# Kernel optimization log

Measured on AMD Instinct MI355X. Metric: run time of the kernel, lower is better.

Reference implementation:

```python
import jax, jax.numpy as jnp
import numpy as np

N_NODES = 50000
N_EDGES = 800000
IN_DIM = 128
HID = 32
HEADS = 4


def _lin_init(key, fan_in, fan_out):
    k1, k2 = jax.random.split(key)
    s = 1.0 / np.sqrt(fan_in)
    W = jax.random.uniform(k1, (fan_in, fan_out), jnp.float32, -s, s)
    b = jax.random.uniform(k2, (fan_out,), jnp.float32, -s, s)
    return W, b


def setup_inputs() -> dict:
    key = jax.random.key(0)
    keys = jax.random.split(key, 12)
    x = jax.random.normal(keys[0], (N_NODES, IN_DIM), jnp.float32)
    edge_index = jax.random.randint(keys[1], (2, N_EDGES), 0, N_NODES, jnp.int64)

    # conv1: in_dim -> heads*hid (128 -> 4*32)
    Wq1, bq1 = _lin_init(keys[2], IN_DIM, HEADS * HID)
    Wk1, bk1 = _lin_init(keys[3], IN_DIM, HEADS * HID)
    Wv1, bv1 = _lin_init(keys[4], IN_DIM, HEADS * HID)
    Ws1, bs1 = _lin_init(keys[5], IN_DIM, HEADS * HID)
    # conv2: 128 -> 1*32
    Wq2, bq2 = _lin_init(keys[6], HEADS * HID, HID)
    Wk2, bk2 = _lin_init(keys[7], HEADS * HID, HID)
    Wv2, bv2 = _lin_init(keys[8], HEADS * HID, HID)
    Ws2, bs2 = _lin_init(keys[9], HEADS * HID, HID)
    # output linear: 32 -> 1
    Wo, bo = _lin_init(keys[10], HID, 1)

    return {
        "x": x, "edge_index": edge_index,
        "Wq1": Wq1, "bq1": bq1, "Wk1": Wk1, "bk1": bk1,
        "Wv1": Wv1, "bv1": bv1, "Ws1": Ws1, "bs1": bs1,
        "Wq2": Wq2, "bq2": bq2, "Wk2": Wk2, "bk2": bk2,
        "Wv2": Wv2, "bv2": bv2, "Ws2": Ws2, "bs2": bs2,
        "Wo": Wo, "bo": bo,
    }


def transformer_conv(x, edge_index, Wq, bq, Wk, bk, Wv, bv, Ws, bs, heads, d):
    # PyG TransformerConv (concat=True, root_weight=True, beta=False, no edge attr).
    n = x.shape[0]
    src, dst = edge_index[0], edge_index[1]  # message j(src) -> i(dst)
    q = (x @ Wq + bq).reshape(n, heads, d)
    k = (x @ Wk + bk).reshape(n, heads, d)
    v = (x @ Wv + bv).reshape(n, heads, d)
    # per-edge attention logits [E, heads]
    logits = (q[dst] * k[src]).sum(-1) / jnp.sqrt(jnp.float32(d))
    # segment softmax over incoming edges of each target node
    m = jax.ops.segment_max(logits, dst, num_segments=n)
    p = jnp.exp(logits - m[dst])
    denom = jax.ops.segment_sum(p, dst, num_segments=n)
    alpha = p / denom[dst]  # [E, heads]
    # weighted scatter-add of values
    msg = alpha[:, :, None] * v[src]  # [E, heads, d]
    aggr = jax.ops.segment_sum(msg, dst, num_segments=n).reshape(n, heads * d)
    return aggr + x @ Ws + bs  # root (skip) connection


def reference(x, edge_index,
              Wq1, bq1, Wk1, bk1, Wv1, bv1, Ws1, bs1,
              Wq2, bq2, Wk2, bk2, Wv2, bv2, Ws2, bs2,
              Wo, bo):
    h = transformer_conv(x, edge_index, Wq1, bq1, Wk1, bk1, Wv1, bv1, Ws1, bs1, HEADS, HID)
    h = jax.nn.relu(h)
    h = transformer_conv(h, edge_index, Wq2, bq2, Wk2, bk2, Wv2, bv2, Ws2, bs2, 1, HID)
    h = jax.nn.relu(h)
    g = h.mean(axis=0)  # [HID]
    return g @ Wo + bo  # [1]
```

## Files before the change

kernel.cpp:

```cpp
#include <hip/hip_runtime.h>
#include <math.h>

#define N_NODES 50000
#define N_EDGES 800000
#define NBK 196
#define BCAP 6144

typedef short short8 __attribute__((ext_vector_type(8)));
typedef float f32x4 __attribute__((ext_vector_type(4)));
typedef float f32x2 __attribute__((ext_vector_type(2)));

__device__ inline unsigned short f2bf(float v) {
  unsigned u = __float_as_uint(v);
  u += 0x7FFFu + ((u >> 16) & 1u);
  return (unsigned short)(u >> 16);
}
__device__ inline float bf2f(unsigned short b) {
  return __uint_as_float(((unsigned)b) << 16);
}
__device__ inline float bflo(unsigned u) { return __uint_as_float(u << 16); }
__device__ inline float bfhi(unsigned u) { return __uint_as_float(u & 0xFFFF0000u); }
__device__ inline unsigned char f2fp8(float v) {
  return (unsigned char)(__builtin_amdgcn_cvt_pk_fp8_f32(v, 0.f, 0, false) & 0xFF);
}
template <bool HI>
__device__ inline f32x2 fp8dec(unsigned u) {
  return __builtin_amdgcn_cvt_pk_f32_fp8(u, HI);
}

#define SCL 0.17677669529663687f

#define CAST_B 6250
#define C1_B 256
#define C2_B 64
__global__ void prep_fused(const float* __restrict__ x,
                           const float* __restrict__ Wq1, const float* __restrict__ Wk1,
                           const float* __restrict__ Wv1, const float* __restrict__ Ws1,
                           const float* __restrict__ bq1, const float* __restrict__ bk1,
                           const float* __restrict__ bv1, const float* __restrict__ bs1,
                           const float* __restrict__ Wq2, const float* __restrict__ Wk2,
                           const float* __restrict__ Wv2, const float* __restrict__ Ws2,
                           const float* __restrict__ bq2, const float* __restrict__ bk2,
                           const float* __restrict__ bv2, const float* __restrict__ bs2,
                           unsigned short* __restrict__ xb, unsigned short* __restrict__ Wt1,
                           float* __restrict__ bcat1, unsigned short* __restrict__ Wt2,
                           float* __restrict__ bcat2, int* __restrict__ bhist,
                           float* __restrict__ ACC) {
  const int b = blockIdx.x, tid = threadIdx.x;
  if (b < CAST_B) {
    int i = b * 256 + tid;
    float4 v = ((const float4*)x)[i];
    ushort4 o;
    o.x = f2bf(v.x); o.y = f2bf(v.y); o.z = f2bf(v.z); o.w = f2bf(v.w);
    ((ushort4*)xb)[i] = o;
  } else if (b < CAST_B + C1_B) {
    int i = (b - CAST_B) * 256 + tid;
    int c = i >> 7, k = i & 127;
    int mi = c >> 7, lc = c & 127;
    const float* W = (mi == 0) ? Wq1 : (mi == 1) ? Wk1 : (mi == 2) ? Wv1 : Ws1;
    float scl = (mi == 0) ? SCL : 1.f;
    Wt1[i] = f2bf(W[(size_t)k * 128 + lc] * scl);
    if (i < 512) {
      int bm = i >> 7, bl = i & 127;
      const float* bb = (bm == 0) ? bq1 : (bm == 1) ? bk1 : (bm == 2) ? bv1 : bs1;
      bcat1[i] = bb[bl] * ((bm == 0) ? SCL : 1.f);
    }
  } else if (b < CAST_B + C1_B + C2_B) {
    int i = (b - CAST_B - C1_B) * 256 + tid;
    int c = i >> 7, k = i & 127;
    int mi = c >> 5, lc = c & 31;
    const float* W = (mi == 0) ? Wq2 : (mi == 1) ? Wk2 : (mi == 2) ? Wv2 : Ws2;
    float scl = (mi == 0) ? SCL : 1.f;
    Wt2[i] = f2bf(W[(size_t)k * 32 + lc] * scl);
    if (i < 128) {
      int bm = i >> 5, bl = i & 31;
      const float* bb = (bm == 0) ? bq2 : (bm == 1) ? bk2 : (bm == 2) ? bv2 : bs2;
      bcat2[i] = bb[bl] * ((bm == 0) ? SCL : 1.f);
    }
  } else {
    if (tid < NBK) bhist[tid] = 0;
    else if (tid >= 224 && tid < 256) ACC[tid - 224] = 0.f;
  }
}

__global__ __launch_bounds__(256) void gemm_conv1(
    const unsigned short* __restrict__ Ab, const unsigned short* __restrict__ Wt,
    const float* __restrict__ bcat, unsigned short* __restrict__ Q1b,
    unsigned short* __restrict__ SK1, unsigned char* __restrict__ KV8, int M) {
  __shared__ __align__(16) unsigned char Lsb[64 * 272];
  unsigned short* Ls16 = (unsigned short*)Lsb;
  const int bm = blockIdx.x * 64;
  const int tid = threadIdx.x, wave = tid >> 6, lane = tid & 63;
  const int lr = lane & 15, q = lane >> 4;

  if (blockIdx.y < 2) {
    const int coloff = blockIdx.y ? 384 : 0;
    unsigned short* out = blockIdx.y ? SK1 : Q1b;
    f32x4 acc[4][2];
#pragma unroll
    for (int i = 0; i < 4; ++i)
#pragma unroll
      for (int j = 0; j < 2; ++j) acc[i][j] = (f32x4){0.f, 0.f, 0.f, 0.f};
#pragma unroll
    for (int ks = 0; ks < 4; ++ks) {
      short8 af[4], bf[2];
#pragma unroll
      for (int i = 0; i < 4; ++i) {
        int gm = bm + i * 16 + lr; if (gm >= M) gm = 0;
        af[i] = *(const short8*)(Ab + (size_t)gm * 128 + ks * 32 + q * 8);
      }
#pragma unroll
      for (int j = 0; j < 2; ++j)
        bf[j] = *(const short8*)(Wt + (size_t)(coloff + wave * 32 + j * 16 + lr) * 128 + ks * 32 + q * 8);
#pragma unroll
      for (int i = 0; i < 4; ++i)
#pragma unroll
        for (int j = 0; j < 2; ++j)
          acc[i][j] = __builtin_amdgcn_mfma_f32_16x16x32_bf16(af[i], bf[j], acc[i][j], 0, 0, 0);
    }
    float bj[2];
#pragma unroll
    for (int j = 0; j < 2; ++j) bj[j] = bcat[coloff + wave * 32 + j * 16 + lr];
#pragma unroll
    for (int i = 0; i < 4; ++i)
#pragma unroll
      for (int r = 0; r < 4; ++r) {
        int row = i * 16 + q * 4 + r;
#pragma unroll
        for (int j = 0; j < 2; ++j) {
          int c = wave * 32 + j * 16 + lr;
          Ls16[row * 136 + c] = f2bf(acc[i][j][r] + bj[j]);
        }
      }
    __syncthreads();
#pragma unroll
    for (int p = 0; p < 8; ++p) {
      int idx = tid + p * 256;
      int row = idx >> 5, u = idx & 31;
      int gr = bm + row;
      if (gr < M) *(uint2*)(out + (size_t)gr * 128 + u * 4) = *(const uint2*)&Ls16[row * 136 + u * 4];
    }
  } else {
    f32x4 acc[4][4];
#pragma unroll
    for (int i = 0; i < 4; ++i)
#pragma unroll
      for (int j = 0; j < 4; ++j) acc[i][j] = (f32x4){0.f, 0.f, 0.f, 0.f};
#pragma unroll
    for (int ks = 0; ks < 4; ++ks) {
      short8 af[4], bf[4];
#pragma unroll
      for (int i = 0; i < 4; ++i) {
        int gm = bm + i * 16 + lr; if (gm >= M) gm = 0;
        af[i] = *(const short8*)(Ab + (size_t)gm * 128 + ks * 32 + q * 8);
      }
#pragma unroll
      for (int j = 0; j < 4; ++j)
        bf[j] = *(const short8*)(Wt + (size_t)(128 + wave * 64 + j * 16 + lr) * 128 + ks * 32 + q * 8);
#pragma unroll
      for (int i = 0; i < 4; ++i)
#pragma unroll
        for (int j = 0; j < 4; ++j)
          acc[i][j] = __builtin_amdgcn_mfma_f32_16x16x32_bf16(af[i], bf[j], acc[i][j], 0, 0, 0);
    }
    float bj[4];
#pragma unroll
    for (int j = 0; j < 4; ++j) bj[j] = bcat[128 + wave * 64 + j * 16 + lr];
#pragma unroll
    for (int i = 0; i < 4; ++i)
#pragma unroll
      for (int r = 0; r < 4; ++r) {
        int row = i * 16 + q * 4 + r;
#pragma unroll
        for (int j = 0; j < 4; ++j) {
          int c = wave * 64 + j * 16 + lr;
          int bslot = (c < 128) ? (4 * (c >> 1) + (c & 1))
                                : (4 * ((c - 128) >> 1) + 2 + ((c - 128) & 1));
          Lsb[row * 272 + bslot] = f2fp8(acc[i][j][r] + bj[j]);
        }
      }
    __syncthreads();
#pragma unroll
    for (int p = 0; p < 16; ++p) {
      int idx = tid + p * 256;
      int row = idx >> 6, u = idx & 63;
      int gr = bm + row;
      if (gr < M) *(unsigned*)(KV8 + (size_t)gr * 256 + u * 4) = *(const unsigned*)&Lsb[row * 272 + u * 4];
    }
  }
}

__global__ __launch_bounds__(256) void gemm2(
    const unsigned short* __restrict__ Ab, const unsigned short* __restrict__ Wt,
    const float* __restrict__ bcat, unsigned char* __restrict__ C2b, int M) {
  __shared__ __align__(16) unsigned char Lsb[64 * 272];
  const int bm = blockIdx.x * 64;
  const int tid = threadIdx.x, wave = tid >> 6, lane = tid & 63;
  const int lr = lane & 15, q = lane >> 4;

  f32x4 acc[4][2];
#pragma unroll
  for (int i = 0; i < 4; ++i)
#pragma unroll
    for (int j = 0; j < 2; ++j) acc[i][j] = (f32x4){0.f, 0.f, 0.f, 0.f};

#pragma unroll
  for (int ks = 0; ks < 4; ++ks) {
    short8 af[4], bf[2];
#pragma unroll
    for (int i = 0; i < 4; ++i) {
      int gm = bm + i * 16 + lr; if (gm >= M) gm = 0;
      af[i] = *(const short8*)(Ab + (size_t)gm * 128 + ks * 32 + q * 8);
    }
#pragma unroll
    for (int j = 0; j < 2; ++j)
      bf[j] = *(const short8*)(Wt + (size_t)(wave * 32 + j * 16 + lr) * 128 + ks * 32 + q * 8);
#pragma unroll
    for (int i = 0; i < 4; ++i)
#pragma unroll
      for (int j = 0; j < 2; ++j)
        acc[i][j] = __builtin_amdgcn_mfma_f32_16x16x32_bf16(af[i], bf[j], acc[i][j], 0, 0, 0);
  }

  float bj[2];
#pragma unroll
  for (int j = 0; j < 2; ++j) bj[j] = bcat[wave * 32 + j * 16 + lr];
#pragma unroll
  for (int i = 0; i < 4; ++i)
#pragma unroll
    for (int r = 0; r < 4; ++r) {
      int row = i * 16 + q * 4 + r;
#pragma unroll
      for (int j = 0; j < 2; ++j) {
        int c = wave * 32 + j * 16 + lr;
        float val = acc[i][j][r] + bj[j];
        if (c < 32) {
          *(unsigned short*)&Lsb[row * 272 + 2 * c] = f2bf(val);
        } else if (c < 64) {
          int d = c - 32;
          Lsb[row * 272 + 64 + 4 * (d >> 1) + (d & 1)] = f2fp8(val);
        } else if (c < 96) {
          int d = c - 64;
          Lsb[row * 272 + 64 + 4 * (d >> 1) + 2 + (d & 1)] = f2fp8(val);
        } else {
          *(unsigned short*)&Lsb[row * 272 + 192 + 2 * (c - 96)] = f2bf(val);
        }
      }
    }
  __syncthreads();
#pragma unroll
  for (int p = 0; p < 16; ++p) {
    int idx = tid + p * 256;
    int row = idx >> 6, u = idx & 63;
    int gr = bm + row;
    if (gr < M) *(unsigned*)(C2b + (size_t)gr * 256 + u * 4) = *(const unsigned*)&Lsb[row * 272 + u * 4];
  }
}

__global__ void bucket_hist(const int* __restrict__ ei, int* __restrict__ bhist, int E) {
  __shared__ int h[NBK];
  for (int i = threadIdx.x; i < NBK; i += 256) h[i] = 0;
  __syncthreads();
  int e = blockIdx.x * 4096 + threadIdx.x;
#pragma unroll
  for (int p = 0; p < 16; ++p, e += 256)
    if (e < E) atomicAdd(&h[ei[E + e] >> 8], 1);
  __syncthreads();
  for (int i = threadIdx.x; i < NBK; i += 256)
    if (h[i]) atomicAdd(&bhist[i], h[i]);
}

__global__ void bucket_scan(const int* __restrict__ bhist, int* __restrict__ boff,
                            int* __restrict__ bcur) {
  __shared__ int s[256];
  int t = threadIdx.x;
  int v = (t < NBK) ? bhist[t] : 0;
  s[t] = v;
  __syncthreads();
#pragma unroll
  for (int off = 1; off < 256; off <<= 1) {
    int u = (t >= off) ? s[t - off] : 0;
    __syncthreads();
    s[t] += u;
    __syncthreads();
  }
  if (t < NBK) {
    int excl = s[t] - v;
    boff[t] = excl;
    bcur[t] = excl;
  }
  if (t == NBK - 1) boff[NBK] = s[t];
}

__global__ void bucket_scatter(const int* __restrict__ ei, int* __restrict__ bcur,
                               int2* __restrict__ ebuck, int E) {
  __shared__ int lh[NBK];
  for (int i = threadIdx.x; i < NBK; i += 256) lh[i] = 0;
  __syncthreads();
  const int e0 = blockIdx.x * 4096;
  int srcs[16], dsts[16];
#pragma unroll
  for (int p = 0; p < 16; ++p) {
    int e = e0 + p * 256 + threadIdx.x;
    if (e < E) {
      srcs[p] = ei[e];
      dsts[p] = ei[E + e];
      atomicAdd(&lh[dsts[p] >> 8], 1);
    } else dsts[p] = -1;
  }
  __syncthreads();
  for (int i = threadIdx.x; i < NBK; i += 256)
    if (lh[i]) lh[i] = atomicAdd(&bcur[i], lh[i]);
  __syncthreads();
#pragma unroll
  for (int p = 0; p < 16; ++p) {
    if (dsts[p] >= 0) {
      int slot = atomicAdd(&lh[dsts[p] >> 8], 1);
      ebuck[slot] = make_int2(srcs[p], dsts[p]);
    }
  }
}

__global__ void bucket_csr(const int2* __restrict__ ebuck, const int* __restrict__ boff,
                           int* __restrict__ rowptr, int* __restrict__ esrc, int N) {
  const int b = blockIdx.x;
  const int lo = boff[b], hi = boff[b + 1];
  const int cnt = hi - lo;
  __shared__ int hist[256];
  __shared__ int cur[256];
  __shared__ int sorted[BCAP];
  const int t = threadIdx.x;
  hist[t] = 0;
  __syncthreads();
  for (int i = t; i < cnt; i += 256) {
    int2 ed = ebuck[lo + i];
    atomicAdd(&hist[ed.y & 255], 1);
  }
  __syncthreads();
  int v = hist[t];
  sorted[t] = v;
  __syncthreads();
#pragma unroll
  for (int off = 1; off < 256; off <<= 1) {
    int u = (t >= off) ? sorted[t - off] : 0;
    __syncthreads();
    sorted[t] += u;
    __syncthreads();
  }
  int excl = sorted[t] - v;
  cur[t] = excl;
  int node = b * 256 + t;
  if (node <= N) rowptr[node] = lo + excl;
  __syncthreads();
  for (int i = t; i < cnt; i += 256) {
    int2 ed = ebuck[lo + i];
    int slot = atomicAdd(&cur[ed.y & 255], 1);
    if (slot < BCAP) sorted[slot] = ed.x;
    else esrc[lo + slot] = ed.x << 8;
  }
  __syncthreads();
  int lim = cnt < BCAP ? cnt : BCAP;
  for (int i = t; i < lim; i += 256) esrc[lo + i] = sorted[i] << 8;
}

__global__ void node_attn1(const int* __restrict__ rowptr, const int* __restrict__ esrc,
                           const unsigned short* __restrict__ Qb,
                           const unsigned char* __restrict__ KV8,
                           const unsigned short* __restrict__ SK, unsigned short* __restrict__ Hb,
                           int n) {
  int node = (blockIdx.x * blockDim.x + threadIdx.x) >> 6;
  int lane = threadIdx.x & 63;
  if (node >= n) return;
  const int half = lane >> 5, ll = lane & 31;
  const int r0 = rowptr[node], r1 = rowptr[node + 1];
  uint2 qq = *(const uint2*)(Qb + (size_t)node * 128 + ll * 4);
  const float q0 = bflo(qq.x), q1 = bfhi(qq.x), q2 = bflo(qq.y), q3 = bfhi(qq.y);
  float l = 0.f, a0 = 0.f, a1 = 0.f, a2 = 0.f, a3 = 0.f;
  const unsigned char* kvb = KV8 + ll * 8;
  int j = r0;
  for (; j + 8 <= r1; j += 8) {
    int e = j + half * 4;
    int s0 = esrc[e], s1 = esrc[e + 1], s2 = esrc[e + 2], s3 = esrc[e + 3];
    uint2 u0 = *(const uint2*)(kvb + s0);
    uint2 u1 = *(const uint2*)(kvb + s1);
    uint2 u2 = *(const uint2*)(kvb + s2);
    uint2 u3 = *(const uint2*)(kvb + s3);
    f32x2 k0a = fp8dec<false>(u0.x), k0b = fp8dec<false>(u0.y);
    f32x2 k1a = fp8dec<false>(u1.x), k1b = fp8dec<false>(u1.y);
    f32x2 k2a = fp8dec<false>(u2.x), k2b = fp8dec<false>(u2.y);
    f32x2 k3a = fp8dec<false>(u3.x), k3b = fp8dec<false>(u3.y);
    float d0 = q0 * k0a.x + q1 * k0a.y + q2 * k0b.x + q3 * k0b.y;
    float d1 = q0 * k1a.x + q1 * k1a.y + q2 * k1b.x + q3 * k1b.y;
    float d2 = q0 * k2a.x + q1 * k2a.y + q2 * k2b.x + q3 * k2b.y;
    float d3 = q0 * k3a.x + q1 * k3a.y + q2 * k3b.x + q3 * k3b.y;
#pragma unroll
    for (int msk = 1; msk <= 4; msk <<= 1) {
      d0 += __shfl_xor(d0, msk);
      d1 += __shfl_xor(d1, msk);
      d2 += __shfl_xor(d2, msk);
      d3 += __shfl_xor(d3, msk);
    }
    float p0 = __expf(d0), p1 = __expf(d1), p2 = __expf(d2), p3 = __expf(d3);
    l += (p0 + p1) + (p2 + p3);
    f32x2 v0a = fp8dec<true>(u0.x), v0b = fp8dec<true>(u0.y);
    f32x2 v1a = fp8dec<true>(u1.x), v1b = fp8dec<true>(u1.y);
    f32x2 v2a = fp8dec<true>(u2.x), v2b = fp8dec<true>(u2.y);
    f32x2 v3a = fp8dec<true>(u3.x), v3b = fp8dec<true>(u3.y);
    a0 += p0 * v0a.x + p1 * v1a.x + p2 * v2a.x + p3 * v3a.x;
    a1 += p0 * v0a.y + p1 * v1a.y + p2 * v2a.y + p3 * v3a.y;
    a2 += p0 * v0b.x + p1 * v1b.x + p2 * v2b.x + p3 * v3b.x;
    a3 += p0 * v0b.y + p1 * v1b.y + p2 * v2b.y + p3 * v3b.y;
  }
  for (; j < r1; j += 4) {
    int eA = j + half * 2, eB = eA + 1;
    bool vA = eA < r1, vB = eB < r1;
    int sA = esrc[vA ? eA : r0];
    int sB = esrc[vB ? eB : r0];
    uint2 ua = *(const uint2*)(kvb + sA);
    uint2 ub = *(const uint2*)(kvb + sB);
    f32x2 ka1 = fp8dec<false>(ua.x), ka2 = fp8dec<false>(ua.y);
    f32x2 kb1 = fp8dec<false>(ub.x), kb2 = fp8dec<false>(ub.y);
    float dA = q0 * ka1.x + q1 * ka1.y + q2 * ka2.x + q3 * ka2.y;
    float dB = q0 * kb1.x + q1 * kb1.y + q2 * kb2.x + q3 * kb2.y;
#pragma unroll
    for (int msk = 1; msk <= 4; msk <<= 1) {
      dA += __shfl_xor(dA, msk);
      dB += __shfl_xor(dB, msk);
    }
    float pA = vA ? __expf(dA) : 0.f;
    float pB = vB ? __expf(dB) : 0.f;
    l += pA + pB;
    f32x2 va1 = fp8dec<true>(ua.x), va2 = fp8dec<true>(ua.y);
    f32x2 vb1 = fp8dec<true>(ub.x), vb2 = fp8dec<true>(ub.y);
    a0 += pA * va1.x + pB * vb1.x;
    a1 += pA * va1.y + pB * vb1.y;
    a2 += pA * va2.x + pB * vb2.x;
    a3 += pA * va2.y + pB * vb2.y;
  }
  l  += __shfl_xor(l, 32);
  a0 += __shfl_xor(a0, 32);
  a1 += __shfl_xor(a1, 32);
  a2 += __shfl_xor(a2, 32);
  a3 += __shfl_xor(a3, 32);
  float inv = (l > 0.f) ? 1.f / l : 0.f;
  if (half == 0) {
    uint2 sk = *(const uint2*)(SK + (size_t)node * 128 + ll * 4);
    float o0 = fmaxf(bflo(sk.x) + a0 * inv, 0.f);
    float o1 = fmaxf(bfhi(sk.x) + a1 * inv, 0.f);
    float o2 = fmaxf(bflo(sk.y) + a2 * inv, 0.f);
    float o3 = fmaxf(bfhi(sk.y) + a3 * inv, 0.f);
    uint2 hb;
    hb.x = ((unsigned)f2bf(o1) << 16) | (unsigned)f2bf(o0);
    hb.y = ((unsigned)f2bf(o3) << 16) | (unsigned)f2bf(o2);
    *(uint2*)(Hb + (size_t)node * 128 + ll * 4) = hb;
  }
}

__global__ void node_attn2(const int* __restrict__ rowptr, const int* __restrict__ esrc,
                           unsigned char* __restrict__ C2b, int n) {
  int node = (blockIdx.x * blockDim.x + threadIdx.x) >> 6;
  int lane = threadIdx.x & 63;
  if (node >= n) return;
  const int g = lane >> 4, gl = lane & 15;
  const int r0 = rowptr[node], r1 = rowptr[node + 1];
  unsigned qu = *(const unsigned*)(C2b + (size_t)node * 256 + gl * 4);
  const float q0 = bflo(qu), q1 = bfhi(qu);
  float l = 0.f, a0 = 0.f, a1 = 0.f;
  const unsigned char* kvb = C2b + 64 + gl * 4;
  int j = r0;
  for (; j + 8 <= r1; j += 8) {
    int e = j + g * 2;
    int s0 = esrc[e], s1 = esrc[e + 1];
    unsigned u0 = *(const unsigned*)(kvb + s0);
    unsigned u1 = *(const unsigned*)(kvb + s1);
    f32x2 k0 = fp8dec<false>(u0), k1 = fp8dec<false>(u1);
    float d0 = q0 * k0.x + q1 * k0.y;
    float d1 = q0 * k1.x + q1 * k1.y;
#pragma unroll
    for (int msk = 1; msk <= 8; msk <<= 1) {
      d0 += __shfl_xor(d0, msk);
      d1 += __shfl_xor(d1, msk);
    }
    float p0 = __expf(d0), p1 = __expf(d1);
    l += p0 + p1;
    f32x2 v0 = fp8dec<true>(u0), v1 = fp8dec<true>(u1);
    a0 += p0 * v0.x + p1 * v1.x;
    a1 += p0 * v0.y + p1 * v1.y;
  }
  for (; j < r1; j += 4) {
    bool v = (j + g) < r1;
    int s = esrc[v ? j + g : r0];
    unsigned u = *(const unsigned*)(kvb + s);
    f32x2 kd = fp8dec<false>(u);
    float d = q0 * kd.x + q1 * kd.y;
#pragma unroll
    for (int msk = 1; msk <= 8; msk <<= 1) d += __shfl_xor(d, msk);
    float p = v ? __expf(d) : 0.f;
    l += p;
    f32x2 vd = fp8dec<true>(u);
    a0 += p * vd.x;
    a1 += p * vd.y;
  }
#pragma unroll
  for (int msk = 16; msk <= 32; msk <<= 1) {
    l  += __shfl_xor(l, msk);
    a0 += __shfl_xor(a0, msk);
    a1 += __shfl_xor(a1, msk);
  }
  float inv = (l > 0.f) ? 1.f / l : 0.f;
  if (lane < 16) {
    unsigned* h = (unsigned*)(C2b + (size_t)node * 256 + 192 + gl * 4);
    unsigned hu = *h;
    float o0 = bflo(hu) + a0 * inv;
    float o1 = bfhi(hu) + a1 * inv;
    *h = ((unsigned)f2bf(o1) << 16) | (unsigned)f2bf(o0);
  }
}

__global__ void mean_reduce(const unsigned char* __restrict__ C2b, float* __restrict__ ACC, int n) {
  __shared__ float s[256];
  float acc = 0.f;
  int stride = gridDim.x * blockDim.x;
  int total = n * 32;
  for (int i = blockIdx.x * blockDim.x + threadIdx.x; i < total; i += stride) {
    int node = i >> 5, c = i & 31;
    unsigned short h = *(const unsigned short*)(C2b + (size_t)node * 256 + 192 + c * 2);
    acc += fmaxf(bf2f(h), 0.f);
  }
  s[threadIdx.x] = acc;
  __syncthreads();
  for (int off = 128; off >= 32; off >>= 1) {
    if (threadIdx.x < off) s[threadIdx.x] += s[threadIdx.x + off];
    __syncthreads();
  }
  if (threadIdx.x < 32) atomicAdd(&ACC[threadIdx.x], s[threadIdx.x]);
}

__global__ void final_out(const float* __restrict__ ACC, const float* __restrict__ Wo,
                          const float* __restrict__ bo, float* __restrict__ out, float invN) {
  int lane = threadIdx.x;
  float v = 0.f;
  if (lane < 32) v = ACC[lane] * invN * Wo[lane];
  v += __shfl_xor(v, 1);
  v += __shfl_xor(v, 2);
  v += __shfl_xor(v, 4);
  v += __shfl_xor(v, 8);
  v += __shfl_xor(v, 16);
  v += __shfl_xor(v, 32);
  if (lane == 0) out[0] = v + bo[0];
}

extern "C" void kernel_launch(void* const* d_in, const int* in_sizes, int n_in,
                              void* d_out, int out_size, void* d_ws, size_t ws_size,
                              hipStream_t stream) {
  const float* x   = (const float*)d_in[0];
  const int*   ei  = (const int*)d_in[1];
  const float* Wq1 = (const float*)d_in[2];  const float* bq1 = (const float*)d_in[3];
  const float* Wk1 = (const float*)d_in[4];  const float* bk1 = (const float*)d_in[5];
  const float* Wv1 = (const float*)d_in[6];  const float* bv1 = (const float*)d_in[7];
  const float* Ws1 = (const float*)d_in[8];  const float* bs1 = (const float*)d_in[9];
  const float* Wq2 = (const float*)d_in[10]; const float* bq2 = (const float*)d_in[11];
  const float* Wk2 = (const float*)d_in[12]; const float* bk2 = (const float*)d_in[13];
  const float* Wv2 = (const float*)d_in[14]; const float* bv2 = (const float*)d_in[15];
  const float* Ws2 = (const float*)d_in[16]; const float* bs2 = (const float*)d_in[17];
  const float* Wo  = (const float*)d_in[18]; const float* bo  = (const float*)d_in[19];

  char* ws = (char*)d_ws;
  const int N = N_NODES, E = N_EDGES;
  const int GB = (N + 63) / 64;
  const int EB = (E + 4095) / 4096;

  unsigned short* xb  = (unsigned short*)(ws + 0);
  unsigned short* Q1b = (unsigned short*)(ws + 12800000);
  unsigned short* SK1 = (unsigned short*)(ws + 25600000);
  unsigned char*  KV1 = (unsigned char*)(ws + 38400000);
  unsigned short* H1b = (unsigned short*)(ws + 64000000);
  unsigned char*  C2  = (unsigned char*)(ws + 76800000);
  int* rowptr = (int*)(ws + 102400000);
  int* esrc   = (int*)(ws + 102700032);
  int* bhist  = (int*)(ws + 105900032);
  int* boff   = (int*)(ws + 105901056);
  int* bcur   = (int*)(ws + 105902080);
  unsigned short* Wt1   = (unsigned short*)(ws + 105903104);
  unsigned short* Wt2   = (unsigned short*)(ws + 106034176);
  float*          bcat1 = (float*)(ws + 106066944);
  float*          bcat2 = (float*)(ws + 106068992);
  float*          ACC   = (float*)(ws + 106069504);
  int2*           ebuck = (int2*)(ws + 106070016);

  float* out = (float*)d_out;

  dim3 blk(256);

  prep_fused<<<dim3(CAST_B + C1_B + C2_B + 1), blk, 0, stream>>>(
      x, Wq1, Wk1, Wv1, Ws1, bq1, bk1, bv1, bs1,
      Wq2, Wk2, Wv2, Ws2, bq2, bk2, bv2, bs2,
      xb, Wt1, bcat1, Wt2, bcat2, bhist, ACC);

  bucket_hist<<<dim3(EB), blk, 0, stream>>>(ei, bhist, E);
  bucket_scan<<<dim3(1), blk, 0, stream>>>(bhist, boff, bcur);
  bucket_scatter<<<dim3(EB), blk, 0, stream>>>(ei, bcur, ebuck, E);
  bucket_csr<<<dim3(NBK), blk, 0, stream>>>(ebuck, boff, rowptr, esrc, N);

  gemm_conv1<<<dim3(GB, 3), blk, 0, stream>>>(xb, Wt1, bcat1, Q1b, SK1, KV1, N);

  node_attn1<<<dim3((N * 64 + 255) / 256), blk, 0, stream>>>(rowptr, esrc, Q1b, KV1, SK1, H1b, N);

  gemm2<<<dim3(GB), blk, 0, stream>>>(H1b, Wt2, bcat2, C2, N);

  node_attn2<<<dim3((N * 64 + 255) / 256), blk, 0, stream>>>(rowptr, esrc, C2, N);

  mean_reduce<<<dim3(1024), blk, 0, stream>>>(C2, ACC, N);
  final_out<<<dim3(1), dim3(64), 0, stream>>>(ACC, Wo, bo, out, 1.0f / (float)N);
}
```

Before: 284.3 us.

## Merge conv1 GEMM column blocks into one block and stage A tile in LDS

The conv1 projection GEMM now runs one block per 64-row tile instead of three blocks along y. Each wave computes 128 output columns (Q, K, V or skip), and the A tile is loaded once into shared memory and reused across all 512 columns. The conv2 GEMM stages its A tile in LDS the same way. This removes repeated global reads of x rows and widens the output stores, at the cost of more accumulator registers per wave (32 f32x4), roughly three times the LDS per block, and a third as many blocks.

Measured after the change: 270.4 us. 4.9% less time.

```diff
diff --git a/kernel.cpp b/kernel.cpp
--- a/kernel.cpp
+++ b/kernel.cpp
@@ -87,105 +87,86 @@
     const unsigned short* __restrict__ Ab, const unsigned short* __restrict__ Wt,
     const float* __restrict__ bcat, unsigned short* __restrict__ Q1b,
     unsigned short* __restrict__ SK1, unsigned char* __restrict__ KV8, int M) {
-  __shared__ __align__(16) unsigned char Lsb[64 * 272];
-  unsigned short* Ls16 = (unsigned short*)Lsb;
+  __shared__ __align__(16) unsigned char L[3][64 * 272];
+  unsigned short* As = (unsigned short*)L[0];
   const int bm = blockIdx.x * 64;
   const int tid = threadIdx.x, wave = tid >> 6, lane = tid & 63;
   const int lr = lane & 15, q = lane >> 4;
 
-  if (blockIdx.y < 2) {
-    const int coloff = blockIdx.y ? 384 : 0;
-    unsigned short* out = blockIdx.y ? SK1 : Q1b;
-    f32x4 acc[4][2];
+#pragma unroll
+  for (int p = 0; p < 4; ++p) {
+    int f = tid + p * 256;
+    int row = f >> 4, chunk = f & 15;
+    int gm = bm + row; if (gm >= M) gm = 0;
+    uint4 v = *(const uint4*)(Ab + (size_t)gm * 128 + chunk * 8);
+    *(uint4*)&As[row * 136 + chunk * 8] = v;
+  }
+  __syncthreads();
+
+  const int colbase = wave * 128;
+  f32x4 acc[4][8];
+#pragma unroll
+  for (int i = 0; i < 4; ++i)
+#pragma unroll
+    for (int j = 0; j < 8; ++j) acc[i][j] = (f32x4){0.f, 0.f, 0.f, 0.f};
+
+#pragma unroll
+  for (int ks = 0; ks < 4; ++ks) {
+    short8 af[4];
 #pragma unroll
     for (int i = 0; i < 4; ++i)
-#pragma unroll
-      for (int j = 0; j < 2; ++j) acc[i][j] = (f32x4){0.f, 0.f, 0.f, 0.f};
-#pragma unroll
-    for (int ks = 0; ks < 4; ++ks) {
-      short8 af[4], bf[2];
-#pragma unroll
-      for (int i = 0; i < 4; ++i) {
-        int gm = bm + i * 16 + lr; if (gm >= M) gm = 0;
-        af[i] = *(const short8*)(Ab + (size_t)gm * 128 + ks * 32 + q * 8);
-      }
-#pragma unroll
-      for (int j = 0; j < 2; ++j)
-        bf[j] = *(const short8*)(Wt + (size_t)(coloff + wave * 32 + j * 16 + lr) * 128 + ks * 32 + q * 8);
+      af[i] = *(short8*)&As[(i * 16 + lr) * 136 + ks * 32 + q * 8];
+#pragma unroll
+    for (int j = 0; j < 8; ++j) {
+      short8 bf = *(const short8*)(Wt + (size_t)(colbase + j * 16 + lr) * 128 + ks * 32 + q * 8);
 #pragma unroll
       for (int i = 0; i < 4; ++i)
-#pragma unroll
-        for (int j = 0; j < 2; ++j)
-          acc[i][j] = __builtin_amdgcn_mfma_f32_16x16x32_bf16(af[i], bf[j], acc[i][j], 0, 0, 0);
-    }
-    float bj[2];
-#pragma unroll
-    for (int j = 0; j < 2; ++j) bj[j] = bcat[coloff + wave * 32 + j * 16 + lr];
+        acc[i][j] = __builtin_amdgcn_mfma_f32_16x16x32_bf16(af[i], bf, acc[i][j], 0, 0, 0);
+    }
+  }
+  __syncthreads();
+
+  float bj[8];
+#pragma unroll
+  for (int j = 0; j < 8; ++j) bj[j] = bcat[colbase + j * 16 + lr];
+
+  if (wave == 0 || wave == 3) {
+    unsigned short* Ls16 = (unsigned short*)((wave == 0) ? L[1] : L[0]);
 #pragma unroll
     for (int i = 0; i < 4; ++i)
 #pragma unroll
       for (int r = 0; r < 4; ++r) {
         int row = i * 16 + q * 4 + r;
 #pragma unroll
-        for (int j = 0; j < 2; ++j) {
-          int c = wave * 32 + j * 16 + lr;
-          Ls16[row * 136 + c] = f2bf(acc[i][j][r] + bj[j]);
+        for (int j = 0; j < 8; ++j)
+          Ls16[row * 136 + j * 16 + lr] = f2bf(acc[i][j][r] + bj[j]);
+      }
+  } else {
+    unsigned char* KLs = L[2];
+    const int voff = (wave == 2) ? 2 : 0;
+#pragma unroll
+    for (int i = 0; i < 4; ++i)
+#pragma unroll
+      for (int r = 0; r < 4; ++r) {
+        int row = i * 16 + q * 4 + r;
+#pragma unroll
+        for (int j = 0; j < 8; ++j) {
+          int d = j * 16 + lr;
+          KLs[row * 272 + 4 * (d >> 1) + voff + (d & 1)] = f2fp8(acc[i][j][r] + bj[j]);
         }
       }
-    __syncthreads();
-#pragma unroll
-    for (int p = 0; p < 8; ++p) {
-      int idx = tid + p * 256;
-      int row = idx >> 5, u = idx & 31;
-      int gr = bm + row;
-      if (gr < M) *(uint2*)(out + (size_t)gr * 128 + u * 4) = *(const uint2*)&Ls16[row * 136 + u * 4];
-    }
-  } else {
-    f32x4 acc[4][4];
-#pragma unroll
-    for (int i = 0; i < 4; ++i)
-#pragma unroll
-      for (int j = 0; j < 4; ++j) acc[i][j] = (f32x4){0.f, 0.f, 0.f, 0.f};
-#pragma unroll
-    for (int ks = 0; ks < 4; ++ks) {
-      short8 af[4], bf[4];
-#pragma unroll
-      for (int i = 0; i < 4; ++i) {
-        int gm = bm + i * 16 + lr; if (gm >= M) gm = 0;
-        af[i] = *(const short8*)(Ab + (size_t)gm * 128 + ks * 32 + q * 8);
-      }
-#pragma unroll
-      for (int j = 0; j < 4; ++j)
-        bf[j] = *(const short8*)(Wt + (size_t)(128 + wave * 64 + j * 16 + lr) * 128 + ks * 32 + q * 8);
-#pragma unroll
-      for (int i = 0; i < 4; ++i)
-#pragma unroll
-        for (int j = 0; j < 4; ++j)
-          acc[i][j] = __builtin_amdgcn_mfma_f32_16x16x32_bf16(af[i], bf[j], acc[i][j], 0, 0, 0);
-    }
-    float bj[4];
-#pragma unroll
-    for (int j = 0; j < 4; ++j) bj[j] = bcat[128 + wave * 64 + j * 16 + lr];
-#pragma unroll
-    for (int i = 0; i < 4; ++i)
-#pragma unroll
-      for (int r = 0; r < 4; ++r) {
-        int row = i * 16 + q * 4 + r;
-#pragma unroll
-        for (int j = 0; j < 4; ++j) {
-          int c = wave * 64 + j * 16 + lr;
-          int bslot = (c < 128) ? (4 * (c >> 1) + (c & 1))
-                                : (4 * ((c - 128) >> 1) + 2 + ((c - 128) & 1));
-          Lsb[row * 272 + bslot] = f2fp8(acc[i][j][r] + bj[j]);
-        }
-      }
-    __syncthreads();
-#pragma unroll
-    for (int p = 0; p < 16; ++p) {
-      int idx = tid + p * 256;
-      int row = idx >> 6, u = idx & 63;
-      int gr = bm + row;
-      if (gr < M) *(unsigned*)(KV8 + (size_t)gr * 256 + u * 4) = *(const unsigned*)&Lsb[row * 272 + u * 4];
+  }
+  __syncthreads();
+
+#pragma unroll
+  for (int p = 0; p < 4; ++p) {
+    int f = tid + p * 256;
+    int row = f >> 4, u = f & 15;
+    int gr = bm + row;
+    if (gr < M) {
+      *(uint4*)(Q1b + (size_t)gr * 128 + u * 8) = *(uint4*)&((unsigned short*)L[1])[row * 136 + u * 8];
+      *(uint4*)(KV8 + (size_t)gr * 256 + u * 16) = *(uint4*)&L[2][row * 272 + u * 16];
+      *(uint4*)(SK1 + (size_t)gr * 128 + u * 8) = *(uint4*)&((unsigned short*)L[0])[row * 136 + u * 8];
     }
   }
 }
@@ -193,11 +174,22 @@
 __global__ __launch_bounds__(256) void gemm2(
     const unsigned short* __restrict__ Ab, const unsigned short* __restrict__ Wt,
     const float* __restrict__ bcat, unsigned char* __restrict__ C2b, int M) {
+  __shared__ __align__(16) unsigned short As[64 * 136];
   __shared__ __align__(16) unsigned char Lsb[64 * 272];
   const int bm = blockIdx.x * 64;
   const int tid = threadIdx.x, wave = tid >> 6, lane = tid & 63;
   const int lr = lane & 15, q = lane >> 4;
 
+#pragma unroll
+  for (int p = 0; p < 4; ++p) {
+    int f = tid + p * 256;
+    int row = f >> 4, chunk = f & 15;
+    int gm = bm + row; if (gm >= M) gm = 0;
+    uint4 v = *(const uint4*)(Ab + (size_t)gm * 128 + chunk * 8);
+    *(uint4*)&As[row * 136 + chunk * 8] = v;
+  }
+  __syncthreads();
+
   f32x4 acc[4][2];
 #pragma unroll
   for (int i = 0; i < 4; ++i)
@@ -206,20 +198,17 @@
 
 #pragma unroll
   for (int ks = 0; ks < 4; ++ks) {
-    short8 af[4], bf[2];
-#pragma unroll
-    for (int i = 0; i < 4; ++i) {
-      int gm = bm + i * 16 + lr; if (gm >= M) gm = 0;
-      af[i] = *(const short8*)(Ab + (size_t)gm * 128 + ks * 32 + q * 8);
-    }
-#pragma unroll
-    for (int j = 0; j < 2; ++j)
-      bf[j] = *(const short8*)(Wt + (size_t)(wave * 32 + j * 16 + lr) * 128 + ks * 32 + q * 8);
+    short8 af[4];
 #pragma unroll
     for (int i = 0; i < 4; ++i)
-#pragma unroll
-      for (int j = 0; j < 2; ++j)
-        acc[i][j] = __builtin_amdgcn_mfma_f32_16x16x32_bf16(af[i], bf[j], acc[i][j], 0, 0, 0);
+      af[i] = *(short8*)&As[(i * 16 + lr) * 136 + ks * 32 + q * 8];
+#pragma unroll
+    for (int j = 0; j < 2; ++j) {
+      short8 bf = *(const short8*)(Wt + (size_t)(wave * 32 + j * 16 + lr) * 128 + ks * 32 + q * 8);
+#pragma unroll
+      for (int i = 0; i < 4; ++i)
+        acc[i][j] = __builtin_amdgcn_mfma_f32_16x16x32_bf16(af[i], bf, acc[i][j], 0, 0, 0);
+    }
   }
 
   float bj[2];
@@ -602,7 +591,7 @@
   bucket_scatter<<<dim3(EB), blk, 0, stream>>>(ei, bcur, ebuck, E);
   bucket_csr<<<dim3(NBK), blk, 0, stream>>>(ebuck, boff, rowptr, esrc, N);
 
-  gemm_conv1<<<dim3(GB, 3), blk, 0, stream>>>(xb, Wt1, bcat1, Q1b, SK1, KV1, N);
+  gemm_conv1<<<dim3(GB), blk, 0, stream>>>(xb, Wt1, bcat1, Q1b, SK1, KV1, N);
 
   node_attn1<<<dim3((N * 64 + 255) / 256), blk, 0, stream>>>(rowptr, esrc, Q1b, KV1, SK1, H1b, N);
 
```
